# Kernel optimization log

Hardware: AMD Instinct MI355X
Metric: run time of the kernel (lower is better)

Reference implementation:

```python
import jax, jax.numpy as jnp
import numpy as np

B, W, H, V, L = 64, 512, 1024, 32000, 2


def setup_inputs() -> dict:
    key = jax.random.key(0)
    ks = jax.random.split(key, 20)
    s = 0.02  # init scale
    n = lambda k, shp: jax.random.normal(k, shp, jnp.float32)
    return {
        "input": jax.random.randint(ks[0], (B, 1), 0, V),
        "h0": n(ks[1], (L, B, H)),
        "c0": n(ks[2], (L, B, H)),
        "encoder_output": n(ks[3], (B, W, H)),
        "embedding": n(ks[4], (V, H)) * s,
        "W_ih0": n(ks[5], (4 * H, H)) * s,
        "W_hh0": n(ks[6], (4 * H, H)) * s,
        "b_ih0": n(ks[7], (4 * H,)) * s,
        "b_hh0": n(ks[8], (4 * H,)) * s,
        "W_ih1": n(ks[9], (4 * H, H)) * s,
        "W_hh1": n(ks[10], (4 * H, H)) * s,
        "b_ih1": n(ks[11], (4 * H,)) * s,
        "b_hh1": n(ks[12], (4 * H,)) * s,
        "att_w": n(ks[13], (2 * H,)) * s,
        "att_b": n(ks[14], (1,)) * s,
        "input_W": n(ks[15], (H, 2 * H)) * s,
        "input_b": n(ks[16], (H,)) * s,
        "out_W": n(ks[17], (V, H)) * s,
        "out_b": n(ks[18], (V,)) * s,
    }


def _lstm_step(x, h, c, W_ih, W_hh, b_ih, b_hh):
    # PyTorch gate order: i, f, g, o
    g = x @ W_ih.T + h @ W_hh.T + b_ih + b_hh
    i, f, gg, o = jnp.split(g, 4, axis=-1)
    c2 = jax.nn.sigmoid(f) * c + jax.nn.sigmoid(i) * jnp.tanh(gg)
    return jax.nn.sigmoid(o) * jnp.tanh(c2), c2


def reference(input, h0, c0, encoder_output, embedding,
              W_ih0, W_hh0, b_ih0, b_hh0, W_ih1, W_hh1, b_ih1, b_hh1,
              att_w, att_b, input_W, input_b, out_W, out_b):
    Hd = h0.shape[-1]
    emb = embedding[input]                       # (B,1,H)
    att_state = h0[-1] * c0[-1]                  # (B,H)
    # Vectorized replacement of the per-word cat+linear loop:
    # att_line(cat(enc_w, att_state)) = enc_w @ w_enc + att_state @ w_st + b
    w_enc, w_st = att_w[:Hd], att_w[Hd:]
    scores = encoder_output @ w_enc + (att_state @ w_st)[:, None] + att_b[0]  # (B,W)
    # Original quirk: weigth starts with a zeros column, then softmax over
    # weigth[:, 0:-1] -> zero column + scores for words 0..W-2 (last dropped).
    zeros = jnp.zeros((scores.shape[0], 1), scores.dtype)
    full = jnp.concatenate([zeros, scores[:, :-1]], axis=1)  # (B,W)
    wts = jax.nn.softmax(full, axis=1)
    ctx = jnp.einsum('bw,bwh->bh', wts, encoder_output)      # (B,H)
    x = jnp.concatenate([ctx, emb[:, 0, :]], axis=-1)        # (B,2H)
    x = x @ input_W.T + input_b                              # (B,H)
    h1, c1 = _lstm_step(x, h0[0], c0[0], W_ih0, W_hh0, b_ih0, b_hh0)
    h2, c2 = _lstm_step(h1, h0[1], c0[1], W_ih1, W_hh1, b_ih1, b_hh1)
    logits = h2 @ out_W.T + out_b                            # (B,V)
    logp = jax.nn.log_softmax(logits, axis=-1)[:, None, :]   # (B,1,V)
    return logp, jnp.stack([h1, h2]), jnp.stack([c1, c2])
```

## Files before the change

kernel.cpp:

```cpp
#include <hip/hip_runtime.h>
#include <hip/hip_bf16.h>

#define Bsz 64
#define Wln 512
#define Hd  1024
#define Vc  32000

typedef short v8s __attribute__((ext_vector_type(8)));
typedef float f32x4 __attribute__((ext_vector_type(4)));

__device__ inline unsigned short f2b(float f) {
  union { float f; unsigned u; } v; v.f = f;
  return (unsigned short)((v.u + 0x8000u) >> 16);
}
__device__ inline float wave_sum(float v) {
  #pragma unroll
  for (int o = 32; o; o >>= 1) v += __shfl_down(v, o);
  return v;
}
__device__ inline float wave_max(float v) {
  #pragma unroll
  for (int o = 32; o; o >>= 1) v = fmaxf(v, __shfl_down(v, o));
  return v;
}
__device__ inline float sigm(float x) { return 1.f / (1.f + expf(-x)); }

__device__ inline v8s cvt_frag(float4 x0, float4 x1) {
  v8s r;
  r[0] = (short)f2b(x0.x); r[1] = (short)f2b(x0.y);
  r[2] = (short)f2b(x0.z); r[3] = (short)f2b(x0.w);
  r[4] = (short)f2b(x1.x); r[5] = (short)f2b(x1.y);
  r[6] = (short)f2b(x1.z); r[7] = (short)f2b(x1.w);
  return r;
}

__global__ __launch_bounds__(256) void k_satt_emb(
    const float* __restrict__ h0, const float* __restrict__ c0,
    const float* __restrict__ att_w, const float* __restrict__ att_b,
    const int* __restrict__ input, const float* __restrict__ emb,
    float* __restrict__ s_att, float* __restrict__ cat)
{
  int b = blockIdx.x, t = threadIdx.x;
  int idx = input[b];
  for (int j = t; j < Hd; j += 256)
    cat[b * 2 * Hd + Hd + j] = emb[(size_t)idx * Hd + j];
  size_t base = (size_t)(Bsz + b) * Hd;
  float s = 0.f;
  for (int j = t; j < Hd; j += 256)
    s += h0[base + j] * c0[base + j] * att_w[Hd + j];
  s = wave_sum(s);
  __shared__ float red[4];
  if ((t & 63) == 0) red[t >> 6] = s;
  __syncthreads();
  if (t == 0) s_att[b] = red[0] + red[1] + red[2] + red[3] + att_b[0];
}

__global__ __launch_bounds__(256) void k_scores(
    const float* __restrict__ enc, const float* __restrict__ att_w,
    const float* __restrict__ s_att, float* __restrict__ scores)
{
  int row = blockIdx.x * 4 + (threadIdx.x >> 6);
  int lane = threadIdx.x & 63;
  const float* p = enc + (size_t)row * Hd + lane * 16;
  const float* w = att_w + lane * 16;
  float s = 0.f;
  #pragma unroll
  for (int c = 0; c < 4; ++c) {
    float4 e = *(const float4*)(p + c * 4);
    float4 ww = *(const float4*)(w + c * 4);
    s += e.x * ww.x + e.y * ww.y + e.z * ww.z + e.w * ww.w;
  }
  s = wave_sum(s);
  if (lane == 0) scores[row] = s + s_att[row >> 9];
}

__global__ __launch_bounds__(512) void k_softmax(
    const float* __restrict__ scores, float* __restrict__ wts)
{
  int b = blockIdx.x, t = threadIdx.x;
  float v = (t == 0) ? 0.f : scores[b * Wln + t - 1];
  __shared__ float redm[8], reds[8];
  float m = wave_max(v);
  if ((t & 63) == 0) redm[t >> 6] = m;
  __syncthreads();
  m = redm[0];
  #pragma unroll
  for (int i = 1; i < 8; ++i) m = fmaxf(m, redm[i]);
  float e = expf(v - m);
  float s = wave_sum(e);
  if ((t & 63) == 0) reds[t >> 6] = s;
  __syncthreads();
  s = reds[0];
  #pragma unroll
  for (int i = 1; i < 8; ++i) s += reds[i];
  wts[b * Wln + t] = e / s;
}

__global__ __launch_bounds__(256) void k_ctx_part(
    const float* __restrict__ wts, const float* __restrict__ enc,
    float* __restrict__ part)
{
  int b = blockIdx.x >> 3, ch = blockIdx.x & 7;
  int t = threadIdx.x;
  __shared__ float w[64];
  if (t < 64) w[t] = wts[b * Wln + ch * 64 + t];
  __syncthreads();
  int h4 = t * 4;
  const float* p = enc + (size_t)b * Wln * Hd + (size_t)ch * 64 * Hd + h4;
  float a0 = 0, a1 = 0, a2 = 0, a3 = 0;
  #pragma unroll 4
  for (int i = 0; i < 64; ++i) {
    float4 e = *(const float4*)(p + (size_t)i * Hd);
    float wi = w[i];
    a0 += wi * e.x; a1 += wi * e.y; a2 += wi * e.z; a3 += wi * e.w;
  }
  float* o = part + ((size_t)b * 8 + ch) * Hd + h4;
  o[0] = a0; o[1] = a1; o[2] = a2; o[3] = a3;
}

__global__ __launch_bounds__(256) void k_ctx_red(
    const float* __restrict__ part, float* __restrict__ cat)
{
  int idx = blockIdx.x * 256 + threadIdx.x;
  int b = idx >> 10, h = idx & 1023;
  float s = 0.f;
  #pragma unroll
  for (int c = 0; c < 8; ++c) s += part[((size_t)b * 8 + c) * Hd + h];
  cat[b * 2 * Hd + h] = s;
}

template<int NS>
__global__ __launch_bounds__(512) void gemm_v4(
    const float* __restrict__ A1, const float* __restrict__ A1b, int sA1,
    const float* __restrict__ B1, int sB1, const float* __restrict__ bias1,
    float* __restrict__ out1,
    const float* __restrict__ A2, const float* __restrict__ A2b, int sA2,
    const float* __restrict__ B2, int sB2, const float* __restrict__ bias2,
    float* __restrict__ out2,
    int N, int nblk1)
{
  constexpr int KS  = 8 / NS;
  constexpr int KSL = 1024 / KS;
  const int tid = threadIdx.x;

  const float *A, *Ab, *B, *bias; float* out; int sA, sB, bid;
  if ((int)blockIdx.x < nblk1) {
    A = A1; Ab = A1b; sA = sA1; B = B1; sB = sB1; bias = bias1; out = out1;
    bid = blockIdx.x;
  } else {
    A = A2; Ab = A2b; sA = sA2; B = B2; sB = sB2; bias = bias2; out = out2;
    bid = blockIdx.x - nblk1;
  }

  __shared__ __align__(16) char pool[131072];

  #pragma unroll
  for (int it = 0; it < 16; ++it) {
    int idx = it * 512 + tid;
    int row = idx >> 7, ch = idx & 127;
    const float* src = A + (size_t)row * sA + ch * 8;
    float4 x0 = *(const float4*)src;
    float4 x1 = *(const float4*)(src + 4);
    if (Ab) {
      const float* s2 = Ab + (size_t)row * sA + ch * 8;
      float4 y0 = *(const float4*)s2;
      float4 y1 = *(const float4*)(s2 + 4);
      x0.x += y0.x; x0.y += y0.y; x0.z += y0.z; x0.w += y0.w;
      x1.x += y1.x; x1.y += y1.y; x1.z += y1.z; x1.w += y1.w;
    }
    *(v8s*)(pool + row * 2048 + ((ch * 16) ^ ((row & 7) << 4))) = cvt_frag(x0, x1);
  }
  __syncthreads();

  const int w = tid >> 6, lane = tid & 63;
  const int r = lane & 15, q = lane >> 4;
  const int nsub = w % NS, kh = w / NS;
  const int n0 = bid * (NS * 16);

  f32x4 acc[4] = {{0,0,0,0},{0,0,0,0},{0,0,0,0},{0,0,0,0}};
  const float* bp = B + (size_t)(n0 + nsub * 16 + r) * sB + kh * KSL + q * 8;
  const int swz = (r & 7) << 4;

  #pragma unroll 4
  for (int kk = 0; kk < KSL / 32; ++kk) {
    float4 b0 = *(const float4*)(bp + kk * 32);
    float4 b1 = *(const float4*)(bp + kk * 32 + 4);
    v8s bf = cvt_frag(b0, b1);
    int cb = ((kh * KSL + kk * 32 + q * 8) * 2) ^ swz;
    #pragma unroll
    for (int m = 0; m < 4; ++m) {
      v8s af = *(const v8s*)(pool + (m * 16 + r) * 2048 + cb);
      acc[m] = __builtin_amdgcn_mfma_f32_16x16x32_bf16(af, bf, acc[m], 0, 0, 0);
    }
  }

  __syncthreads();
  float (*red)[64][17] = (float(*)[64][17])pool;
  #pragma unroll
  for (int m = 0; m < 4; ++m)
    #pragma unroll
    for (int rr = 0; rr < 4; ++rr)
      red[w][lane][m * 4 + rr] = acc[m][rr];
  __syncthreads();

  constexpr int COLS = NS * 16;
  #pragma unroll
  for (int it = 0; it < NS * 2; ++it) {
    int e = it * 512 + tid;
    int cc = e % COLS, rowi = e / COLS;
    int ns2 = cc >> 4, lo = cc & 15;
    int idx = ((rowi >> 4) << 2) + (rowi & 3);
    int le  = (((rowi >> 2) & 3) << 4) + lo;
    float s = 0.f;
    #pragma unroll
    for (int j = 0; j < KS; ++j) s += red[ns2 + j * NS][le][idx];
    float bb = bias ? bias[n0 + cc] : 0.f;
    out[(size_t)rowi * N + n0 + cc] = s + bb;
  }
}

__global__ __launch_bounds__(256) void k_lstm(
    const float* __restrict__ g1, const float* __restrict__ g2,
    const float* __restrict__ c0,
    float* __restrict__ out_h, float* __restrict__ out_c)
{
  int b = blockIdx.x >> 2;
  int j = ((blockIdx.x & 3) << 8) + threadIdx.x;
  const float* ga = g1 + (size_t)b * 4 * Hd;
  const float* gb = g2 + (size_t)b * 4 * Hd;
  float gi = ga[j] + gb[j];
  float gf = ga[Hd + j] + gb[Hd + j];
  float gg = ga[2 * Hd + j] + gb[2 * Hd + j];
  float go = ga[3 * Hd + j] + gb[3 * Hd + j];
  float c = sigm(gf) * c0[(size_t)b * Hd + j] + sigm(gi) * tanhf(gg);
  float h = sigm(go) * tanhf(c);
  out_h[b * Hd + j] = h;
  out_c[b * Hd + j] = c;
}

__global__ __launch_bounds__(1024) void k_logsoftmax(float* __restrict__ lg)
{
  int b = blockIdx.x, t = threadIdx.x;
  float* row = lg + (size_t)b * Vc;
  __shared__ float red[16];
  float m = -1e30f;
  for (int w = t; w < Vc; w += 1024) m = fmaxf(m, row[w]);
  m = wave_max(m);
  if ((t & 63) == 0) red[t >> 6] = m;
  __syncthreads();
  float M = red[0];
  #pragma unroll
  for (int i = 1; i < 16; ++i) M = fmaxf(M, red[i]);
  __syncthreads();
  float s = 0.f;
  for (int w = t; w < Vc; w += 1024) s += expf(row[w] - M);
  s = wave_sum(s);
  if ((t & 63) == 0) red[t >> 6] = s;
  __syncthreads();
  float S = red[0];
  #pragma unroll
  for (int i = 1; i < 16; ++i) S += red[i];
  float lse = M + logf(S);
  for (int w = t; w < Vc; w += 1024) row[w] = row[w] - lse;
}

extern "C" void kernel_launch(void* const* d_in, const int* in_sizes, int n_in,
                              void* d_out, int out_size, void* d_ws, size_t ws_size,
                              hipStream_t stream)
{
  const int*   input = (const int*)d_in[0];
  const float* h0    = (const float*)d_in[1];
  const float* c0    = (const float*)d_in[2];
  const float* enc   = (const float*)d_in[3];
  const float* emb   = (const float*)d_in[4];
  const float* W_ih0 = (const float*)d_in[5];
  const float* W_hh0 = (const float*)d_in[6];
  const float* b_ih0 = (const float*)d_in[7];
  const float* b_hh0 = (const float*)d_in[8];
  const float* W_ih1 = (const float*)d_in[9];
  const float* W_hh1 = (const float*)d_in[10];
  const float* b_ih1 = (const float*)d_in[11];
  const float* b_hh1 = (const float*)d_in[12];
  const float* att_w = (const float*)d_in[13];
  const float* att_b = (const float*)d_in[14];
  const float* inW   = (const float*)d_in[15];
  const float* inb   = (const float*)d_in[16];
  const float* outW  = (const float*)d_in[17];
  const float* outb  = (const float*)d_in[18];
  float* out = (float*)d_out;

  char* sc = (char*)d_out;
  float* g1     = (float*)(sc + 0);
  float* g2     = (float*)(sc + 1048576);
  float* ctxp   = (float*)(sc + 2097152);
  float* cat    = (float*)(sc + 4194304);
  float* x1     = (float*)(sc + 4718592);
  float* x2     = (float*)(sc + 4980736);
  float* scores = (float*)(sc + 5242880);
  float* s_att  = (float*)(sc + 5373952);

  float* out_h = out + (size_t)Bsz * Vc;
  float* out_c = out_h + 2 * Bsz * Hd;
  float* h1 = out_h;
  float* h2 = out_h + Bsz * Hd;

  k_satt_emb<<<Bsz, 256, 0, stream>>>(h0, c0, att_w, att_b, input, emb, s_att, cat);
  k_scores<<<Bsz * Wln / 4, 256, 0, stream>>>(enc, att_w, s_att, scores);
  k_softmax<<<Bsz, 512, 0, stream>>>(scores, scores);
  k_ctx_part<<<Bsz * 8, 256, 0, stream>>>(scores, enc, ctxp);
  k_ctx_red<<<Bsz * Hd / 256, 256, 0, stream>>>(ctxp, cat);

  gemm_v4<1><<<128, 512, 0, stream>>>(
      cat,        nullptr, 2 * Hd, inW,      2 * Hd, inb,     x1,
      cat + Hd,   nullptr, 2 * Hd, inW + Hd, 2 * Hd, nullptr, x2,
      Hd, 64);

  gemm_v4<2><<<256, 512, 0, stream>>>(
      x1, x2,      Hd, W_ih0, Hd, b_ih0, g1,
      h0, nullptr, Hd, W_hh0, Hd, b_hh0, g2,
      4 * Hd, 128);
  k_lstm<<<Bsz * 4, 256, 0, stream>>>(g1, g2, c0, h1, out_c);

  gemm_v4<2><<<256, 512, 0, stream>>>(
      h1,                     nullptr, Hd, W_ih1, Hd, b_ih1, g1,
      h0 + (size_t)Bsz * Hd,  nullptr, Hd, W_hh1, Hd, b_hh1, g2,
      4 * Hd, 128);
  k_lstm<<<Bsz * 4, 256, 0, stream>>>(g1, g2, c0 + (size_t)Bsz * Hd, h2, out_c + Bsz * Hd);

  gemm_v4<4><<<500, 512, 0, stream>>>(
      h2,      nullptr, Hd, outW,    Hd, outb,    out,
      nullptr, nullptr, 0,  nullptr, 0,  nullptr, nullptr,
      Vc, 500);
  k_logsoftmax<<<Bsz, 1024, 0, stream>>>(out);
}
```

Baseline: 149.8 us.

## Fuse attention score and softmax kernels, prefetch GEMM weights into registers

Merges the attention-state reduction and embedding copy into the score kernel, and recomputes the softmax inside the context kernel, removing two launches. The GEMM now loads its weight fragments into registers before staging the activation tile, so global weight latency overlaps the LDS fill; it also adds an occupancy hint. The log-softmax is vectorized with float4 accesses. The register prefetch raises VGPR pressure and could spill under the new launch bound, and each context block recomputes the full softmax redundantly.

Result: no change. 149.2 us (-0.4%).

```diff
diff --git a/kernel.cpp b/kernel.cpp
--- a/kernel.cpp
+++ b/kernel.cpp
@@ -34,85 +34,83 @@
   return r;
 }
 
-__global__ __launch_bounds__(256) void k_satt_emb(
+__global__ __launch_bounds__(256) void k_scores_satt(
+    const float* __restrict__ enc, const float* __restrict__ att_w,
     const float* __restrict__ h0, const float* __restrict__ c0,
-    const float* __restrict__ att_w, const float* __restrict__ att_b,
-    const int* __restrict__ input, const float* __restrict__ emb,
-    float* __restrict__ s_att, float* __restrict__ cat)
-{
-  int b = blockIdx.x, t = threadIdx.x;
-  int idx = input[b];
-  for (int j = t; j < Hd; j += 256)
-    cat[b * 2 * Hd + Hd + j] = emb[(size_t)idx * Hd + j];
-  size_t base = (size_t)(Bsz + b) * Hd;
-  float s = 0.f;
-  for (int j = t; j < Hd; j += 256)
-    s += h0[base + j] * c0[base + j] * att_w[Hd + j];
-  s = wave_sum(s);
+    const float* __restrict__ att_b, const int* __restrict__ input,
+    const float* __restrict__ emb,
+    float* __restrict__ scores, float* __restrict__ s_att,
+    float* __restrict__ cat)
+{
   __shared__ float red[4];
-  if ((t & 63) == 0) red[t >> 6] = s;
-  __syncthreads();
-  if (t == 0) s_att[b] = red[0] + red[1] + red[2] + red[3] + att_b[0];
-}
-
-__global__ __launch_bounds__(256) void k_scores(
-    const float* __restrict__ enc, const float* __restrict__ att_w,
-    const float* __restrict__ s_att, float* __restrict__ scores)
-{
-  int row = blockIdx.x * 4 + (threadIdx.x >> 6);
-  int lane = threadIdx.x & 63;
-  const float* p = enc + (size_t)row * Hd + lane * 16;
-  const float* w = att_w + lane * 16;
-  float s = 0.f;
-  #pragma unroll
-  for (int c = 0; c < 4; ++c) {
-    float4 e = *(const float4*)(p + c * 4);
-    float4 ww = *(const float4*)(w + c * 4);
-    s += e.x * ww.x + e.y * ww.y + e.z * ww.z + e.w * ww.w;
-  }
-  s = wave_sum(s);
-  if (lane == 0) scores[row] = s + s_att[row >> 9];
-}
-
-__global__ __launch_bounds__(512) void k_softmax(
-    const float* __restrict__ scores, float* __restrict__ wts)
-{
-  int b = blockIdx.x, t = threadIdx.x;
-  float v = (t == 0) ? 0.f : scores[b * Wln + t - 1];
-  __shared__ float redm[8], reds[8];
-  float m = wave_max(v);
-  if ((t & 63) == 0) redm[t >> 6] = m;
-  __syncthreads();
-  m = redm[0];
-  #pragma unroll
-  for (int i = 1; i < 8; ++i) m = fmaxf(m, redm[i]);
-  float e = expf(v - m);
-  float s = wave_sum(e);
-  if ((t & 63) == 0) reds[t >> 6] = s;
-  __syncthreads();
-  s = reds[0];
-  #pragma unroll
-  for (int i = 1; i < 8; ++i) s += reds[i];
-  wts[b * Wln + t] = e / s;
+  int t = threadIdx.x;
+  if (blockIdx.x < 8192) {
+    int row = blockIdx.x * 4 + (t >> 6);
+    int lane = t & 63;
+    const float* p = enc + (size_t)row * Hd + lane * 16;
+    const float* w = att_w + lane * 16;
+    float s = 0.f;
+    #pragma unroll
+    for (int c = 0; c < 4; ++c) {
+      float4 e = *(const float4*)(p + c * 4);
+      float4 ww = *(const float4*)(w + c * 4);
+      s += e.x * ww.x + e.y * ww.y + e.z * ww.z + e.w * ww.w;
+    }
+    s = wave_sum(s);
+    if (lane == 0) scores[row] = s;
+  } else {
+    int b = blockIdx.x - 8192;
+    int idx = input[b];
+    for (int j = t; j < Hd; j += 256)
+      cat[b * 2 * Hd + Hd + j] = emb[(size_t)idx * Hd + j];
+    size_t base = (size_t)(Bsz + b) * Hd;
+    float s = 0.f;
+    for (int j = t; j < Hd; j += 256)
+      s += h0[base + j] * c0[base + j] * att_w[Hd + j];
+    s = wave_sum(s);
+    if ((t & 63) == 0) red[t >> 6] = s;
+    __syncthreads();
+    if (t == 0) s_att[b] = red[0] + red[1] + red[2] + red[3] + att_b[0];
+  }
 }
 
 __global__ __launch_bounds__(256) void k_ctx_part(
-    const float* __restrict__ wts, const float* __restrict__ enc,
-    float* __restrict__ part)
+    const float* __restrict__ scores, const float* __restrict__ s_att,
+    const float* __restrict__ enc, float* __restrict__ part)
 {
   int b = blockIdx.x >> 3, ch = blockIdx.x & 7;
   int t = threadIdx.x;
+  float sa = s_att[b];
+  const float* sr = scores + b * Wln;
+  int w0 = t * 2, w1 = t * 2 + 1;
+  float v0 = (w0 == 0) ? 0.f : sr[w0 - 1] + sa;
+  float v1 = sr[w1 - 1] + sa;
+  __shared__ float redm[4], reds[4];
+  float m = fmaxf(v0, v1);
+  m = wave_max(m);
+  if ((t & 63) == 0) redm[t >> 6] = m;
+  __syncthreads();
+  float M = fmaxf(fmaxf(redm[0], redm[1]), fmaxf(redm[2], redm[3]));
+  float e = expf(v0 - M) + expf(v1 - M);
+  e = wave_sum(e);
+  if ((t & 63) == 0) reds[t >> 6] = e;
+  __syncthreads();
+  float S = reds[0] + reds[1] + reds[2] + reds[3];
   __shared__ float w[64];
-  if (t < 64) w[t] = wts[b * Wln + ch * 64 + t];
+  if (t < 64) {
+    int wg = ch * 64 + t;
+    float v = (wg == 0) ? 0.f : sr[wg - 1] + sa;
+    w[t] = expf(v - M) / S;
+  }
   __syncthreads();
   int h4 = t * 4;
   const float* p = enc + (size_t)b * Wln * Hd + (size_t)ch * 64 * Hd + h4;
   float a0 = 0, a1 = 0, a2 = 0, a3 = 0;
   #pragma unroll 4
   for (int i = 0; i < 64; ++i) {
-    float4 e = *(const float4*)(p + (size_t)i * Hd);
+    float4 ev = *(const float4*)(p + (size_t)i * Hd);
     float wi = w[i];
-    a0 += wi * e.x; a1 += wi * e.y; a2 += wi * e.z; a3 += wi * e.w;
+    a0 += wi * ev.x; a1 += wi * ev.y; a2 += wi * ev.z; a3 += wi * ev.w;
   }
   float* o = part + ((size_t)b * 8 + ch) * Hd + h4;
   o[0] = a0; o[1] = a1; o[2] = a2; o[3] = a3;
@@ -130,7 +128,7 @@
 }
 
 template<int NS>
-__global__ __launch_bounds__(512) void gemm_v4(
+__global__ __launch_bounds__(512, 2) void gemm_v6(
     const float* __restrict__ A1, const float* __restrict__ A1b, int sA1,
     const float* __restrict__ B1, int sB1, const float* __restrict__ bias1,
     float* __restrict__ out1,
@@ -141,6 +139,7 @@
 {
   constexpr int KS  = 8 / NS;
   constexpr int KSL = 1024 / KS;
+  constexpr int NCH = KSL / 32;
   const int tid = threadIdx.x;
 
   const float *A, *Ab, *B, *bias; float* out; int sA, sB, bid;
@@ -153,6 +152,19 @@
   }
 
   __shared__ __align__(16) char pool[131072];
+
+  const int w = tid >> 6, lane = tid & 63;
+  const int r = lane & 15, q = lane >> 4;
+  const int nsub = w % NS, kh = w / NS;
+  const int n0 = bid * (NS * 16);
+
+  const float* bp = B + (size_t)(n0 + nsub * 16 + r) * sB + kh * KSL + q * 8;
+  float4 breg[NCH][2];
+  #pragma unroll
+  for (int kk = 0; kk < NCH; ++kk) {
+    breg[kk][0] = *(const float4*)(bp + kk * 32);
+    breg[kk][1] = *(const float4*)(bp + kk * 32 + 4);
+  }
 
   #pragma unroll
   for (int it = 0; it < 16; ++it) {
@@ -172,20 +184,12 @@
   }
   __syncthreads();
 
-  const int w = tid >> 6, lane = tid & 63;
-  const int r = lane & 15, q = lane >> 4;
-  const int nsub = w % NS, kh = w / NS;
-  const int n0 = bid * (NS * 16);
-
   f32x4 acc[4] = {{0,0,0,0},{0,0,0,0},{0,0,0,0},{0,0,0,0}};
-  const float* bp = B + (size_t)(n0 + nsub * 16 + r) * sB + kh * KSL + q * 8;
   const int swz = (r & 7) << 4;
 
-  #pragma unroll 4
-  for (int kk = 0; kk < KSL / 32; ++kk) {
-    float4 b0 = *(const float4*)(bp + kk * 32);
-    float4 b1 = *(const float4*)(bp + kk * 32 + 4);
-    v8s bf = cvt_frag(b0, b1);
+  #pragma unroll
+  for (int kk = 0; kk < NCH; ++kk) {
+    v8s bf = cvt_frag(breg[kk][0], breg[kk][1]);
     int cb = ((kh * KSL + kk * 32 + q * 8) * 2) ^ swz;
     #pragma unroll
     for (int m = 0; m < 4; ++m) {
@@ -244,7 +248,10 @@
   float* row = lg + (size_t)b * Vc;
   __shared__ float red[16];
   float m = -1e30f;
-  for (int w = t; w < Vc; w += 1024) m = fmaxf(m, row[w]);
+  for (int w = t * 4; w < Vc; w += 4096) {
+    float4 v = *(const float4*)(row + w);
+    m = fmaxf(m, fmaxf(fmaxf(v.x, v.y), fmaxf(v.z, v.w)));
+  }
   m = wave_max(m);
   if ((t & 63) == 0) red[t >> 6] = m;
   __syncthreads();
@@ -253,7 +260,10 @@
   for (int i = 1; i < 16; ++i) M = fmaxf(M, red[i]);
   __syncthreads();
   float s = 0.f;
-  for (int w = t; w < Vc; w += 1024) s += expf(row[w] - M);
+  for (int w = t * 4; w < Vc; w += 4096) {
+    float4 v = *(const float4*)(row + w);
+    s += expf(v.x - M) + expf(v.y - M) + expf(v.z - M) + expf(v.w - M);
+  }
   s = wave_sum(s);
   if ((t & 63) == 0) red[t >> 6] = s;
   __syncthreads();
@@ -261,7 +271,11 @@
   #pragma unroll
   for (int i = 1; i < 16; ++i) S += red[i];
   float lse = M + logf(S);
-  for (int w = t; w < Vc; w += 1024) row[w] = row[w] - lse;
+  for (int w = t * 4; w < Vc; w += 4096) {
+    float4 v = *(const float4*)(row + w);
+    v.x -= lse; v.y -= lse; v.z -= lse; v.w -= lse;
+    *(float4*)(row + w) = v;
+  }
 }
 
 extern "C" void kernel_launch(void* const* d_in, const int* in_sizes, int n_in,
@@ -297,37 +311,36 @@
   float* x1     = (float*)(sc + 4718592);
   float* x2     = (float*)(sc + 4980736);
   float* scores = (float*)(sc + 5242880);
-  float* s_att  = (float*)(sc + 5373952);
+  float* s_att  = (float*)(sc + 5505024);
 
   float* out_h = out + (size_t)Bsz * Vc;
   float* out_c = out_h + 2 * Bsz * Hd;
   float* h1 = out_h;
   float* h2 = out_h + Bsz * Hd;
 
-  k_satt_emb<<<Bsz, 256, 0, stream>>>(h0, c0, att_w, att_b, input, emb, s_att, cat);
-  k_scores<<<Bsz * Wln / 4, 256, 0, stream>>>(enc, att_w, s_att, scores);
-  k_softmax<<<Bsz, 512, 0, stream>>>(scores, scores);
-  k_ctx_part<<<Bsz * 8, 256, 0, stream>>>(scores, enc, ctxp);
+  k_scores_satt<<<8256, 256, 0, stream>>>(enc, att_w, h0, c0, att_b, input, emb,
+                                          scores, s_att, cat);
+  k_ctx_part<<<Bsz * 8, 256, 0, stream>>>(scores, s_att, enc, ctxp);
   k_ctx_red<<<Bsz * Hd / 256, 256, 0, stream>>>(ctxp, cat);
 
-  gemm_v4<1><<<128, 512, 0, stream>>>(
-      cat,        nullptr, 2 * Hd, inW,      2 * Hd, inb,     x1,
-      cat + Hd,   nullptr, 2 * Hd, inW + Hd, 2 * Hd, nullptr, x2,
+  gemm_v6<1><<<128, 512, 0, stream>>>(
+      cat,      nullptr, 2 * Hd, inW,      2 * Hd, inb,     x1,
+      cat + Hd, nullptr, 2 * Hd, inW + Hd, 2 * Hd, nullptr, x2,
       Hd, 64);
 
-  gemm_v4<2><<<256, 512, 0, stream>>>(
+  gemm_v6<2><<<256, 512, 0, stream>>>(
       x1, x2,      Hd, W_ih0, Hd, b_ih0, g1,
       h0, nullptr, Hd, W_hh0, Hd, b_hh0, g2,
       4 * Hd, 128);
   k_lstm<<<Bsz * 4, 256, 0, stream>>>(g1, g2, c0, h1, out_c);
 
-  gemm_v4<2><<<256, 512, 0, stream>>>(
+  gemm_v6<2><<<256, 512, 0, stream>>>(
       h1,                     nullptr, Hd, W_ih1, Hd, b_ih1, g1,
       h0 + (size_t)Bsz * Hd,  nullptr, Hd, W_hh1, Hd, b_hh1, g2,
       4 * Hd, 128);
   k_lstm<<<Bsz * 4, 256, 0, stream>>>(g1, g2, c0 + (size_t)Bsz * Hd, h2, out_c + Bsz * Hd);
 
-  gemm_v4<4><<<500, 512, 0, stream>>>(
+  gemm_v6<4><<<500, 512, 0, stream>>>(
       h2,      nullptr, Hd, outW,    Hd, outb,    out,
       nullptr, nullptr, 0,  nullptr, 0,  nullptr, nullptr,
       Vc, 500);
```
